# Performance work log

Hardware: AMD Instinct MI355X
Metric: run time of the kernel (lower is better)

The kernel has to match this reference:

```python
import jax, jax.numpy as jnp
import numpy as np

CHUNK = 16

def setup_inputs() -> dict:
    key = jax.random.key(0)
    k1, k2, k3, k4 = jax.random.split(key, 4)
    B, T, D, N = 2, 2048, 1024, 16
    u_input = jax.random.normal(k1, (B, T, D), dtype=jnp.float32)
    delta = jax.random.uniform(k2, (B, T, D), dtype=jnp.float32)
    b_mat = jax.random.normal(k3, (B, T, D, N), dtype=jnp.float32)
    c_mat = jax.random.normal(k4, (B, T, D, N), dtype=jnp.float32)
    A_log = jnp.log(jnp.linspace(1.0, float(N), N)).astype(jnp.float32)
    return {"u_input": u_input, "delta": delta, "b_mat": b_mat, "c_mat": c_mat, "A_log": A_log}

def reference(u_input, delta, b_mat, c_mat, A_log):
    B, T, D = u_input.shape
    N = A_log.shape[0]
    L = min(CHUNK, T)
    C = T // L  # T chosen divisible by chunk size
    A = -jnp.exp(A_log)  # [N], broadcasts over [B,L,D,N]

    # reshape into chunks and move chunk axis first for lax.scan
    u_c = jnp.moveaxis(u_input.reshape(B, C, L, D), 1, 0)       # [C,B,L,D]
    d_c = jnp.moveaxis(delta.reshape(B, C, L, D), 1, 0)        # [C,B,L,D]
    b_c = jnp.moveaxis(b_mat.reshape(B, C, L, D, N), 1, 0)     # [C,B,L,D,N]
    c_c = jnp.moveaxis(c_mat.reshape(B, C, L, D, N), 1, 0)     # [C,B,L,D,N]

    def step(h, inp):
        u, dl, b, c = inp  # u,dl: [B,L,D]; b,c: [B,L,D,N]; h: [B,D,N]
        deltaA = jnp.clip(dl[..., None] * A, -10.0, 10.0)      # [B,L,D,N]
        eA = jnp.exp(deltaA)
        frac = jnp.where(jnp.abs(deltaA) < 1e-4,
                         dl[..., None],
                         (eA - 1.0) / (A + 1e-12))
        Bu = frac * (b * u[..., None])                          # [B,L,D,N]
        Ah_cum = jnp.cumprod(eA, axis=1)
        h_expand = h[:, None] * Ah_cum                          # [B,L,D,N]
        # flip_weights[t] = eA[t] for t < L-1, and 1 at t = L-1
        fw = jnp.concatenate([eA[:, :-1], jnp.ones_like(eA[:, :1])], axis=1)
        Bu_term = jnp.flip(jnp.cumsum(Bu * fw, axis=1), axis=1)
        h_new = h_expand + Bu_term
        y = (h_new * c).sum(-1)                                 # [B,L,D]
        return h_new[:, -1], y

    h0 = jnp.zeros((B, D, N), dtype=u_input.dtype)
    _, ys = jax.lax.scan(step, h0, (u_c, d_c, b_c, c_c))        # ys: [C,B,L,D]
    return jnp.moveaxis(ys, 0, 1).reshape(B, T, D)
```

## Files before the change

kernel.cpp:

```cpp
#include <hip/hip_runtime.h>

#define BB 2
#define TT 2048
#define DD 1024
#define NN 16
#define LL 16
#define CC (TT / LL)
#define SS 32
#define CPS (CC / SS)

__global__ __launch_bounds__(256, 4) void k1a_segxform(
    const float* __restrict__ delta,
    const float* __restrict__ u,
    const float* __restrict__ bmat,
    const float* __restrict__ A_log,
    float* __restrict__ Pseg,
    float* __restrict__ Qseg)
{
    int g   = blockIdx.x * 256 + threadIdx.x;
    int ng  = g & 7;
    int d   = (g >> 3) & (DD - 1);
    int seg = (g >> 13) & (SS - 1);
    int b   = g >> 18;
    int n0  = ng * 2;

    float A0 = -__expf(A_log[n0]);
    float A1 = -__expf(A_log[n0 + 1]);
    float r0 = 1.0f / (A0 + 1e-12f);
    float r1 = 1.0f / (A1 + 1e-12f);

    float P0 = 1.0f, P1 = 1.0f, Q0 = 0.0f, Q1 = 0.0f;
    int t0seg = seg * (TT / SS);
    for (int c = 0; c < CPS; ++c) {
        int t0   = t0seg + c * LL;
        int base = (b * TT + t0) * DD + d;

        float dl[LL];
        #pragma unroll
        for (int t = 0; t < LL; ++t) dl[t] = delta[base + t * DD];
        float  uu0 = u[base];
        float2 bv  = *reinterpret_cast<const float2*>(&bmat[(long)base * NN + n0]);

        float p0 = 1.0f, p1 = 1.0f, q0 = 0.0f, q1 = 0.0f;
        #pragma unroll
        for (int t = 0; t < LL; ++t) {
            float dA0 = fminf(fmaxf(dl[t] * A0, -10.0f), 10.0f);
            float dA1 = fminf(fmaxf(dl[t] * A1, -10.0f), 10.0f);
            float e0 = __expf(dA0), e1 = __expf(dA1);
            if (t == 0) {
                float f0 = (fabsf(dA0) < 1e-4f) ? dl[t] : (e0 - 1.0f) * r0;
                float f1 = (fabsf(dA1) < 1e-4f) ? dl[t] : (e1 - 1.0f) * r1;
                q0 = f0 * (bv.x * uu0) * e0;
                q1 = f1 * (bv.y * uu0) * e1;
            }
            p0 *= e0; p1 *= e1;
        }
        P0 *= p0; Q0 = Q0 * p0 + q0;
        P1 *= p1; Q1 = Q1 * p1 + q1;
    }
    int oidx = ((b * SS + seg) * DD + d) * NN + n0;
    *reinterpret_cast<float2*>(&Pseg[oidx]) = make_float2(P0, P1);
    *reinterpret_cast<float2*>(&Qseg[oidx]) = make_float2(Q0, Q1);
}

__global__ __launch_bounds__(256) void k1b_scan(
    const float* __restrict__ Pseg,
    const float* __restrict__ Qseg,
    float* __restrict__ hin,
    int S)
{
    int g  = blockIdx.x * 256 + threadIdx.x;
    int dn = g & (DD * NN - 1);
    int b  = g >> 14;

    float h = 0.0f;
    for (int s = 0; s < S; ++s) {
        int idx = (b * S + s) * (DD * NN) + dn;
        hin[idx] = h;
        h = h * Pseg[idx] + Qseg[idx];
    }
}

__global__ __launch_bounds__(256, 4) void k2_main(
    const float* __restrict__ delta,
    const float* __restrict__ u,
    const float* __restrict__ bmat,
    const float* __restrict__ cmat,
    const float* __restrict__ A_log,
    const float* __restrict__ hin,
    float* __restrict__ out)
{
    int g   = blockIdx.x * 256 + threadIdx.x;
    int ng  = g & 7;
    int d   = (g >> 3) & (DD - 1);
    int seg = (g >> 13) & (SS - 1);
    int b   = g >> 18;
    int n0  = ng * 2;

    float A0 = -__expf(A_log[n0]);
    float A1 = -__expf(A_log[n0 + 1]);
    float r0 = 1.0f / (A0 + 1e-12f);
    float r1 = 1.0f / (A1 + 1e-12f);

    float2 hv = *reinterpret_cast<const float2*>(
        &hin[((b * SS + seg) * DD + d) * NN + n0]);
    float h0 = hv.x, h1 = hv.y;

    int t0seg = seg * (TT / SS);
    for (int c = 0; c < CPS; ++c) {
        int  t0    = t0seg + c * LL;
        int  base  = (b * TT + t0) * DD + d;
        long nbase = (long)base * NN + n0;

        float cp0[LL], cp1[LL], g0[LL], g1[LL];
        float pr0 = 1.0f, pr1 = 1.0f;
        #pragma unroll
        for (int t = 0; t < LL; ++t) {
            float  dlv = delta[base + t * DD];
            float  uv  = u[base + t * DD];
            float2 bv  = *reinterpret_cast<const float2*>(
                &bmat[nbase + (long)t * (DD * NN)]);
            float dA0 = fminf(fmaxf(dlv * A0, -10.0f), 10.0f);
            float dA1 = fminf(fmaxf(dlv * A1, -10.0f), 10.0f);
            float e0 = __expf(dA0), e1 = __expf(dA1);
            float f0 = (fabsf(dA0) < 1e-4f) ? dlv : (e0 - 1.0f) * r0;
            float f1 = (fabsf(dA1) < 1e-4f) ? dlv : (e1 - 1.0f) * r1;
            float Bu0 = f0 * (bv.x * uv);
            float Bu1 = f1 * (bv.y * uv);
            pr0 *= e0; pr1 *= e1;
            cp0[t] = pr0; cp1[t] = pr1;
            g0[t] = Bu0 * ((t < LL - 1) ? e0 : 1.0f);
            g1[t] = Bu1 * ((t < LL - 1) ? e1 : 1.0f);
        }

        float cs0 = 0.0f, cs1 = 0.0f;
        #pragma unroll
        for (int k = 0; k < LL; ++k) {
            int t = LL - 1 - k;
            cs0 += g0[k];
            cs1 += g1[k];
            float2 cv = *reinterpret_cast<const float2*>(
                &cmat[nbase + (long)t * (DD * NN)]);
            float v = cv.x * (h0 * cp0[t] + cs0)
                    + cv.y * (h1 * cp1[t] + cs1);
            v += __shfl_xor(v, 1);
            v += __shfl_xor(v, 2);
            v += __shfl_xor(v, 4);
            if (ng == 0) out[base + t * DD] = v;
        }

        h0 = h0 * cp0[LL - 1] + g0[0];
        h1 = h1 * cp1[LL - 1] + g1[0];
    }
}

extern "C" void kernel_launch(void* const* d_in, const int* in_sizes, int n_in,
                              void* d_out, int out_size, void* d_ws, size_t ws_size,
                              hipStream_t stream) {
    (void)in_sizes; (void)n_in; (void)out_size; (void)ws_size;

    const float* u     = (const float*)d_in[0];
    const float* delta = (const float*)d_in[1];
    const float* bmat  = (const float*)d_in[2];
    const float* cmat  = (const float*)d_in[3];
    const float* A_log = (const float*)d_in[4];
    float* out = (float*)d_out;

    size_t tbl = (size_t)BB * SS * DD * NN;
    float* Pseg = (float*)d_ws;
    float* Qseg = Pseg + tbl;
    float* hin  = Qseg + tbl;

    k1a_segxform<<<(BB * SS * DD * (NN / 2)) / 256, 256, 0, stream>>>(
        delta, u, bmat, A_log, Pseg, Qseg);
    k1b_scan<<<(BB * DD * NN) / 256, 256, 0, stream>>>(Pseg, Qseg, hin, SS);
    k2_main<<<(BB * SS * DD * (NN / 2)) / 256, 256, 0, stream>>>(
        delta, u, bmat, cmat, A_log, hin, out);
}
```

Measured before the change: 681.8 us.

## Split chunk processing into two halves to cut register arrays in main kernel

The main kernel now processes each 16-step chunk in two halves of 8. The first half stores cumulative products and prefix sums. The second half computes the remaining exponentials while emitting outputs for both a late and an early timestep. This halves the per-thread register arrays and interleaves compute with the c_mat loads, aiming for better latency hiding. Launch bounds drop to 2 waves per SIMD, which allows more registers per thread but may lower occupancy.

Result: faster. 580.9 us (-14.8%).

```diff
diff --git a/kernel.cpp b/kernel.cpp
--- a/kernel.cpp
+++ b/kernel.cpp
@@ -8,6 +8,7 @@
 #define CC (TT / LL)
 #define SS 32
 #define CPS (CC / SS)
+#define HH 8
 
 __global__ __launch_bounds__(256, 4) void k1a_segxform(
     const float* __restrict__ delta,
@@ -81,7 +82,7 @@
     }
 }
 
-__global__ __launch_bounds__(256, 4) void k2_main(
+__global__ __launch_bounds__(256, 2) void k2_main(
     const float* __restrict__ delta,
     const float* __restrict__ u,
     const float* __restrict__ bmat,
@@ -108,49 +109,71 @@
 
     int t0seg = seg * (TT / SS);
     for (int c = 0; c < CPS; ++c) {
-        int  t0    = t0seg + c * LL;
-        int  base  = (b * TT + t0) * DD + d;
+        int  base  = (b * TT + t0seg + c * LL) * DD + d;
         long nbase = (long)base * NN + n0;
 
-        float cp0[LL], cp1[LL], g0[LL], g1[LL];
-        float pr0 = 1.0f, pr1 = 1.0f;
-        #pragma unroll
-        for (int t = 0; t < LL; ++t) {
-            float  dlv = delta[base + t * DD];
-            float  uv  = u[base + t * DD];
+        float cpA[HH], cpB[HH], pfA[HH], pfB[HH];
+        float pr0 = 1.0f, pr1 = 1.0f, s0 = 0.0f, s1 = 0.0f;
+        #pragma unroll
+        for (int j = 0; j < HH; ++j) {
+            float  dlv = delta[base + j * DD];
+            float  uv  = u[base + j * DD];
             float2 bv  = *reinterpret_cast<const float2*>(
-                &bmat[nbase + (long)t * (DD * NN)]);
+                &bmat[nbase + (long)j * (DD * NN)]);
             float dA0 = fminf(fmaxf(dlv * A0, -10.0f), 10.0f);
             float dA1 = fminf(fmaxf(dlv * A1, -10.0f), 10.0f);
             float e0 = __expf(dA0), e1 = __expf(dA1);
             float f0 = (fabsf(dA0) < 1e-4f) ? dlv : (e0 - 1.0f) * r0;
             float f1 = (fabsf(dA1) < 1e-4f) ? dlv : (e1 - 1.0f) * r1;
-            float Bu0 = f0 * (bv.x * uv);
-            float Bu1 = f1 * (bv.y * uv);
             pr0 *= e0; pr1 *= e1;
-            cp0[t] = pr0; cp1[t] = pr1;
-            g0[t] = Bu0 * ((t < LL - 1) ? e0 : 1.0f);
-            g1[t] = Bu1 * ((t < LL - 1) ? e1 : 1.0f);
+            cpA[j] = pr0; cpB[j] = pr1;
+            s0 += f0 * (bv.x * uv) * e0;
+            s1 += f1 * (bv.y * uv) * e1;
+            pfA[j] = s0; pfB[j] = s1;
         }
 
-        float cs0 = 0.0f, cs1 = 0.0f;
-        #pragma unroll
-        for (int k = 0; k < LL; ++k) {
-            int t = LL - 1 - k;
-            cs0 += g0[k];
-            cs1 += g1[k];
-            float2 cv = *reinterpret_cast<const float2*>(
-                &cmat[nbase + (long)t * (DD * NN)]);
-            float v = cv.x * (h0 * cp0[t] + cs0)
-                    + cv.y * (h1 * cp1[t] + cs1);
-            v += __shfl_xor(v, 1);
-            v += __shfl_xor(v, 2);
-            v += __shfl_xor(v, 4);
-            if (ng == 0) out[base + t * DD] = v;
+        float cs0 = s0, cs1 = s1;
+        #pragma unroll
+        for (int j = 0; j < HH; ++j) {
+            int rr = HH + j;
+            int tl = HH - 1 - j;
+            float  dlv = delta[base + rr * DD];
+            float  uv  = u[base + rr * DD];
+            float2 bv  = *reinterpret_cast<const float2*>(
+                &bmat[nbase + (long)rr * (DD * NN)]);
+            float2 cvh = *reinterpret_cast<const float2*>(
+                &cmat[nbase + (long)rr * (DD * NN)]);
+            float2 cvl = *reinterpret_cast<const float2*>(
+                &cmat[nbase + (long)tl * (DD * NN)]);
+            float dA0 = fminf(fmaxf(dlv * A0, -10.0f), 10.0f);
+            float dA1 = fminf(fmaxf(dlv * A1, -10.0f), 10.0f);
+            float e0 = __expf(dA0), e1 = __expf(dA1);
+            float f0 = (fabsf(dA0) < 1e-4f) ? dlv : (e0 - 1.0f) * r0;
+            float f1 = (fabsf(dA1) < 1e-4f) ? dlv : (e1 - 1.0f) * r1;
+            pr0 *= e0; pr1 *= e1;
+            float fw0 = (rr < LL - 1) ? e0 : 1.0f;
+            float fw1 = (rr < LL - 1) ? e1 : 1.0f;
+            cs0 += f0 * (bv.x * uv) * fw0;
+            cs1 += f1 * (bv.y * uv) * fw1;
+
+            float vhi = cvh.x * (h0 * pr0 + pfA[tl])
+                      + cvh.y * (h1 * pr1 + pfB[tl]);
+            float vlo = cvl.x * (h0 * cpA[tl] + cs0)
+                      + cvl.y * (h1 * cpB[tl] + cs1);
+            vhi += __shfl_xor(vhi, 1);
+            vhi += __shfl_xor(vhi, 2);
+            vhi += __shfl_xor(vhi, 4);
+            vlo += __shfl_xor(vlo, 1);
+            vlo += __shfl_xor(vlo, 2);
+            vlo += __shfl_xor(vlo, 4);
+            if (ng == 0) {
+                out[base + rr * DD] = vhi;
+                out[base + tl * DD] = vlo;
+            }
         }
 
-        h0 = h0 * cp0[LL - 1] + g0[0];
-        h1 = h1 * cp1[LL - 1] + g1[0];
+        h0 = h0 * pr0 + pfA[0];
+        h1 = h1 * pr1 + pfB[0];
     }
 }
 
```
